# Kernel optimization log

Hardware: AMD Instinct MI355X
Metric: run time of the kernel (lower is better)

Reference implementation:

```python
import jax, jax.numpy as jnp
import numpy as np

WS = 7          # window_size
NH = 4          # num_heads
C = 128         # channels
N = WS * WS     # tokens per window = 49
BW = 4096       # number of windows total (batch * windows_per_image)
NW = 64         # windows per image (mask leading dim)


def _rel_pos_index(ws):
    coords = np.stack(np.meshgrid(np.arange(ws), np.arange(ws), indexing='ij'))
    cf = coords.reshape(2, -1)
    rel = (cf[:, :, None] - cf[:, None, :]).transpose(1, 2, 0)
    rel[:, :, 0] += ws - 1
    rel[:, :, 1] += ws - 1
    rel[:, :, 0] *= 2 * ws - 1
    return jnp.asarray(rel.sum(-1).ravel(), dtype=jnp.int32)  # [N*N]


def setup_inputs() -> dict:
    key = jax.random.key(0)
    ks = jax.random.split(key, 6)
    x = jax.random.normal(ks[0], (BW, N, C), dtype=jnp.float32)
    qkv_w = jax.random.normal(ks[1], (C, 3 * C), dtype=jnp.float32) * 0.02
    qkv_b = jnp.zeros((3 * C,), dtype=jnp.float32)
    proj_w = jax.random.normal(ks[2], (C, C), dtype=jnp.float32) * 0.02
    proj_b = jnp.zeros((C,), dtype=jnp.float32)
    bias_table = jax.random.normal(ks[3], ((2 * WS - 1) ** 2, NH), dtype=jnp.float32) * 0.02
    # Swin shifted-window mask: 0 where attention allowed, -100 where blocked
    keep = jax.random.bernoulli(ks[4], 0.5, (NW, N, N))
    mask = jnp.where(keep, 0.0, -100.0).astype(jnp.float32)
    return {"x": x, "qkv_w": qkv_w, "qkv_b": qkv_b, "proj_w": proj_w,
            "proj_b": proj_b, "bias_table": bias_table, "mask": mask}


def reference(x, qkv_w, qkv_b, proj_w, proj_b, bias_table, mask):
    B_, n, c = x.shape
    h = NH
    d = c // h
    scale = d ** -0.5

    qkv = x @ qkv_w + qkv_b                       # [B_, N, 3C]
    qkv = qkv.reshape(B_, n, 3, h, d).transpose(2, 0, 3, 1, 4)  # [3, B_, h, N, d]
    q, k, v = qkv[0], qkv[1], qkv[2]

    attn = jnp.einsum('bhnd,bhmd->bhnm', q * scale, k)          # [B_, h, N, N]

    idx = _rel_pos_index(WS)
    rpb = bias_table[idx].reshape(n, n, h).transpose(2, 0, 1)   # [h, N, N]
    attn = attn + rpb[None]

    nW = mask.shape[0]
    attn = attn.reshape(-1, nW, h, n, n) + mask[None, :, None]  # [B, nW, h, N, N]
    attn = attn.reshape(-1, h, n, n)
    attn = jax.nn.softmax(attn, axis=-1)

    out = jnp.einsum('bhnm,bhmd->bhnd', attn, v)  # [B_, h, N, d]
    out = out.transpose(0, 2, 1, 3).reshape(B_, n, c)
    return out @ proj_w + proj_b
```

## Files before the change

kernel.cpp:

```cpp
#include <hip/hip_runtime.h>

#define NTOK 49
#define CH   128
#define NHEAD 4
#define SCALE 0.17677669529663687f

typedef __bf16 bf16x8 __attribute__((ext_vector_type(8)));
typedef short  s16x8  __attribute__((ext_vector_type(8)));
typedef float  f32x4  __attribute__((ext_vector_type(4)));
typedef s16x8 s16x8_a __attribute__((may_alias));
typedef unsigned short u16_a __attribute__((may_alias));

__device__ __forceinline__ unsigned short f2bf(float f) {
  unsigned int u = __builtin_bit_cast(unsigned int, f);
  u += 0x7FFFu + ((u >> 16) & 1u);
  return (unsigned short)(u >> 16);
}

__device__ __forceinline__ f32x4 mfma_bf16(s16x8 a, s16x8 b, f32x4 c) {
  return __builtin_amdgcn_mfma_f32_16x16x32_bf16(
      __builtin_bit_cast(bf16x8, a), __builtin_bit_cast(bf16x8, b), c, 0, 0, 0);
}

__global__ void prep_kernel(const float* __restrict__ qkv_w,
                            const float* __restrict__ proj_w,
                            const float* __restrict__ bias_table,
                            unsigned short* __restrict__ wT,
                            unsigned short* __restrict__ pT,
                            float* __restrict__ rpb) {
  int t = blockIdx.x * 256 + threadIdx.x;
  if (t < 384 * 128) {
    int n = t >> 7, k = t & 127;
    float v = qkv_w[k * 384 + n];
    if (n < 128) v *= SCALE;
    wT[n * 128 + k] = f2bf(v);
  } else if (t < 384 * 128 + 128 * 128) {
    int u = t - 384 * 128;
    int n = u >> 7, k = u & 127;
    pT[n * 128 + k] = f2bf(proj_w[k * 128 + n]);
  } else if (t < 384 * 128 + 128 * 128 + NHEAD * NTOK * NTOK) {
    int u = t - (384 * 128 + 128 * 128);
    int h = u / (NTOK * NTOK);
    int ij = u % (NTOK * NTOK);
    int i = ij / NTOK, j = ij % NTOK;
    int idx = (i / 7 - j / 7 + 6) * 13 + (i % 7 - j % 7 + 6);
    rpb[h * (NTOK * NTOK) + ij] = bias_table[idx * NHEAD + h];
  }
}

__global__ __launch_bounds__(256, 3)
void attn_fused_kernel(const float* __restrict__ x,
                       const float* __restrict__ qkv_b,
                       const float* __restrict__ proj_b,
                       const float* __restrict__ mask,
                       const unsigned short* __restrict__ wT,
                       const unsigned short* __restrict__ pT,
                       const float* __restrict__ rpb,
                       float* __restrict__ out) {
  __shared__ __align__(16) char smem_raw[54272];
  unsigned short* const smem = (unsigned short*)smem_raw;

  const int w    = blockIdx.x;
  const int tid  = threadIdx.x;
  const int wave = tid >> 6;
  const int lane = tid & 63;
  const int quad = lane >> 4;
  const int l16  = lane & 15;
  const int h    = wave;
  const int wq8  = quad * 8;

  unsigned short* const Xs   = smem;
  unsigned short* const priv = smem + 6656 + wave * 5120;
  unsigned short* const qs   = priv;
  unsigned short* const ks   = priv + 2560;
  unsigned short* const ps   = priv;
  unsigned short* const vt   = priv + 2560;
  unsigned short* const ao   = smem;

  const f32x4 fzero = {0.f, 0.f, 0.f, 0.f};

  {
    const float* xw = x + (size_t)w * (NTOK * CH);
    for (int t = tid; t < NTOK * 32; t += 256) {
      const int row = t >> 5;
      const int c4  = (t & 31) << 2;
      const float4 v = *(const float4*)(xw + row * CH + c4);
      ushort4 pk;
      pk.x = f2bf(v.x); pk.y = f2bf(v.y); pk.z = f2bf(v.z); pk.w = f2bf(v.w);
      *(ushort4*)(Xs + row * 136 + c4) = pk;
    }
  }
  __syncthreads();

  int xrow[4];
#pragma unroll
  for (int mt = 0; mt < 4; ++mt) {
    const int rr = mt * 16 + l16;
    xrow[mt] = (rr < NTOK ? rr : NTOK - 1) * 136;
  }

  f32x4 accq[4][2], acck[4][2];
#pragma unroll
  for (int mt = 0; mt < 4; ++mt)
#pragma unroll
    for (int nt = 0; nt < 2; ++nt) { accq[mt][nt] = fzero; acck[mt][nt] = fzero; }
#pragma unroll
  for (int kt = 0; kt < 4; ++kt) {
    s16x8 a[4], bq[2], bk[2];
#pragma unroll
    for (int mt = 0; mt < 4; ++mt)
      a[mt] = *(const s16x8*)(Xs + xrow[mt] + kt * 32 + wq8);
#pragma unroll
    for (int nt = 0; nt < 2; ++nt) {
      const int rowq = h * 32 + nt * 16 + l16;
      bq[nt] = *(const s16x8*)(wT + (size_t)rowq * 128 + kt * 32 + wq8);
      bk[nt] = *(const s16x8*)(wT + (size_t)(128 + rowq) * 128 + kt * 32 + wq8);
    }
#pragma unroll
    for (int mt = 0; mt < 4; ++mt)
#pragma unroll
      for (int nt = 0; nt < 2; ++nt) {
        accq[mt][nt] = mfma_bf16(a[mt], bq[nt], accq[mt][nt]);
        acck[mt][nt] = mfma_bf16(a[mt], bk[nt], acck[mt][nt]);
      }
  }
#pragma unroll
  for (int nt = 0; nt < 2; ++nt) {
    const int col = nt * 16 + l16;
    const float bq_ = qkv_b[h * 32 + col] * SCALE;
    const float bk_ = qkv_b[128 + h * 32 + col];
#pragma unroll
    for (int mt = 0; mt < 4; ++mt)
#pragma unroll
      for (int r = 0; r < 4; ++r) {
        const int row = mt * 16 + quad * 4 + r;
        *(u16_a*)(qs + row * 40 + col) = f2bf(accq[mt][nt][r] + bq_);
        *(u16_a*)(ks + row * 40 + col) = f2bf(acck[mt][nt][r] + bk_);
      }
  }

  f32x4 accv[4][2];
#pragma unroll
  for (int mt = 0; mt < 4; ++mt)
#pragma unroll
    for (int nt = 0; nt < 2; ++nt) accv[mt][nt] = fzero;
#pragma unroll
  for (int kt = 0; kt < 4; ++kt) {
    s16x8 a[4], bv[2];
#pragma unroll
    for (int mt = 0; mt < 4; ++mt)
      a[mt] = *(const s16x8*)(Xs + xrow[mt] + kt * 32 + wq8);
#pragma unroll
    for (int nt = 0; nt < 2; ++nt)
      bv[nt] = *(const s16x8*)(wT + (size_t)(256 + h * 32 + nt * 16 + l16) * 128 + kt * 32 + wq8);
#pragma unroll
    for (int mt = 0; mt < 4; ++mt)
#pragma unroll
      for (int nt = 0; nt < 2; ++nt)
        accv[mt][nt] = mfma_bf16(a[mt], bv[nt], accv[mt][nt]);
  }

  s16x8 qf[4], kf[4];
#pragma unroll
  for (int t4 = 0; t4 < 4; ++t4) {
    qf[t4] = *(const s16x8_a*)(qs + (t4 * 16 + l16) * 40 + wq8);
    kf[t4] = *(const s16x8_a*)(ks + (t4 * 16 + l16) * 40 + wq8);
  }
  asm volatile("s_waitcnt lgkmcnt(0)" ::: "memory");

#pragma unroll
  for (int nt = 0; nt < 2; ++nt) {
    const float bv_ = qkv_b[256 + h * 32 + nt * 16 + l16];
#pragma unroll
    for (int mt = 0; mt < 4; ++mt)
#pragma unroll
      for (int r = 0; r < 4; ++r) {
        const int row = mt * 16 + quad * 4 + r;
        const int col = nt * 16 + l16;
        *(u16_a*)(vt + col * 72 + row) = f2bf(accv[mt][nt][r] + bv_);
      }
  }

  f32x4 s[4][4];
#pragma unroll
  for (int mt = 0; mt < 4; ++mt)
#pragma unroll
    for (int nt = 0; nt < 4; ++nt)
      s[mt][nt] = mfma_bf16(qf[mt], kf[nt], fzero);

  const float* maskw = mask + (size_t)(w & 63) * (NTOK * NTOK);
  const float* rpbh  = rpb + h * (NTOK * NTOK);
  float rinv[4][4];
  unsigned int pHold[4][4];
#pragma unroll
  for (int mt = 0; mt < 4; ++mt) {
#pragma unroll
    for (int r = 0; r < 4; ++r) {
      const int i = mt * 16 + quad * 4 + r;
      float vals[4];
      float vmax = -1e30f;
#pragma unroll
      for (int nt = 0; nt < 4; ++nt) {
        const int j = nt * 16 + l16;
        float v = -1e30f;
        if (i < NTOK && j < NTOK) {
          const int ij = i * NTOK + j;
          v = s[mt][nt][r] + rpbh[ij] + maskw[ij];
        }
        vals[nt] = v;
        vmax = fmaxf(vmax, v);
      }
#pragma unroll
      for (int off = 1; off < 16; off <<= 1)
        vmax = fmaxf(vmax, __shfl_xor(vmax, off, 64));
      float rsum = 0.f;
#pragma unroll
      for (int nt = 0; nt < 4; ++nt) {
        const float e = __expf(vals[nt] - vmax);
        vals[nt] = e;
        rsum += e;
      }
#pragma unroll
      for (int off = 1; off < 16; off <<= 1)
        rsum += __shfl_xor(rsum, off, 64);
      rinv[mt][r] = 1.f / rsum;
      *(u16_a*)(ps + i * 40 + l16)      = f2bf(vals[0]);
      *(u16_a*)(ps + i * 40 + 16 + l16) = f2bf(vals[1]);
      pHold[mt][r] = (unsigned int)f2bf(vals[2]) | ((unsigned int)f2bf(vals[3]) << 16);
    }
  }

  f32x4 o[4][2];
#pragma unroll
  for (int mt = 0; mt < 4; ++mt)
#pragma unroll
    for (int nt = 0; nt < 2; ++nt) o[mt][nt] = fzero;
  {
    s16x8 pf[4], vf[2];
#pragma unroll
    for (int mt = 0; mt < 4; ++mt)
      pf[mt] = *(const s16x8_a*)(ps + (mt * 16 + l16) * 40 + wq8);
#pragma unroll
    for (int nt = 0; nt < 2; ++nt)
      vf[nt] = *(const s16x8_a*)(vt + (nt * 16 + l16) * 72 + wq8);
#pragma unroll
    for (int mt = 0; mt < 4; ++mt)
#pragma unroll
      for (int nt = 0; nt < 2; ++nt)
        o[mt][nt] = mfma_bf16(pf[mt], vf[nt], o[mt][nt]);
  }
  asm volatile("" ::: "memory");
#pragma unroll
  for (int mt = 0; mt < 4; ++mt)
#pragma unroll
    for (int r = 0; r < 4; ++r) {
      const int i = mt * 16 + quad * 4 + r;
      *(u16_a*)(ps + i * 40 + l16)      = (unsigned short)(pHold[mt][r] & 0xFFFFu);
      *(u16_a*)(ps + i * 40 + 16 + l16) = (unsigned short)(pHold[mt][r] >> 16);
    }
  asm volatile("" ::: "memory");
  {
    s16x8 pf[4], vf[2];
#pragma unroll
    for (int mt = 0; mt < 4; ++mt)
      pf[mt] = *(const s16x8_a*)(ps + (mt * 16 + l16) * 40 + wq8);
#pragma unroll
    for (int nt = 0; nt < 2; ++nt)
      vf[nt] = *(const s16x8_a*)(vt + (nt * 16 + l16) * 72 + 32 + wq8);
#pragma unroll
    for (int mt = 0; mt < 4; ++mt)
#pragma unroll
      for (int nt = 0; nt < 2; ++nt)
        o[mt][nt] = mfma_bf16(pf[mt], vf[nt], o[mt][nt]);
  }

  __syncthreads();
#pragma unroll
  for (int mt = 0; mt < 4; ++mt)
#pragma unroll
    for (int nt = 0; nt < 2; ++nt)
#pragma unroll
      for (int r = 0; r < 4; ++r) {
        const int row = mt * 16 + quad * 4 + r;
        *(u16_a*)(ao + row * 136 + h * 32 + nt * 16 + l16) = f2bf(o[mt][nt][r] * rinv[mt][r]);
      }
  __syncthreads();

  f32x4 po[4][2];
#pragma unroll
  for (int mt = 0; mt < 4; ++mt)
#pragma unroll
    for (int nt = 0; nt < 2; ++nt) po[mt][nt] = fzero;
#pragma unroll
  for (int kt = 0; kt < 4; ++kt) {
    s16x8 a[4], b[2];
#pragma unroll
    for (int mt = 0; mt < 4; ++mt)
      a[mt] = *(const s16x8_a*)(ao + (mt * 16 + l16) * 136 + kt * 32 + wq8);
#pragma unroll
    for (int nt = 0; nt < 2; ++nt)
      b[nt] = *(const s16x8*)(pT + (size_t)(h * 32 + nt * 16 + l16) * 128 + kt * 32 + wq8);
#pragma unroll
    for (int mt = 0; mt < 4; ++mt)
#pragma unroll
      for (int nt = 0; nt < 2; ++nt)
        po[mt][nt] = mfma_bf16(a[mt], b[nt], po[mt][nt]);
  }
  float* outw = out + (size_t)w * (NTOK * CH);
#pragma unroll
  for (int nt = 0; nt < 2; ++nt) {
    const int col = h * 32 + nt * 16 + l16;
    const float pb = proj_b[col];
#pragma unroll
    for (int mt = 0; mt < 4; ++mt)
#pragma unroll
      for (int r = 0; r < 4; ++r) {
        const int row = mt * 16 + quad * 4 + r;
        if (row < NTOK) outw[row * CH + col] = po[mt][nt][r] + pb;
      }
  }
}

extern "C" void kernel_launch(void* const* d_in, const int* in_sizes, int n_in,
                              void* d_out, int out_size, void* d_ws, size_t ws_size,
                              hipStream_t stream) {
  (void)in_sizes; (void)n_in; (void)out_size; (void)ws_size;
  const float* x          = (const float*)d_in[0];
  const float* qkv_w      = (const float*)d_in[1];
  const float* qkv_b      = (const float*)d_in[2];
  const float* proj_w     = (const float*)d_in[3];
  const float* proj_b     = (const float*)d_in[4];
  const float* bias_table = (const float*)d_in[5];
  const float* mask       = (const float*)d_in[6];
  float* out = (float*)d_out;

  unsigned short* wT = (unsigned short*)d_ws;
  unsigned short* pT = wT + 384 * 128;
  float* rpb = (float*)(pT + 128 * 128);

  const int prep_items = 384 * 128 + 128 * 128 + NHEAD * NTOK * NTOK;
  prep_kernel<<<(prep_items + 255) / 256, 256, 0, stream>>>(qkv_w, proj_w, bias_table,
                                                            wT, pT, rpb);
  attn_fused_kernel<<<4096, 256, 0, stream>>>(x, qkv_b, proj_b, mask, wT, pT, rpb, out);
}
```

Baseline: 323.2 us.

## Compute Q and K projections sequentially sharing one LDS staging buffer

Splits the fused Q/K projection loop into two passes. Q is staged through LDS and read into registers first, then K reuses the same LDS region, so each wave's private scratch shrinks and the block's shared memory drops. It also lowers peak accumulator register pressure, since only one set of accumulators is live at a time. Explicit waitcnt and sched_barrier calls are added to order LDS reuse safely, which serialises some work and limits scheduler overlap.

```diff
diff --git a/kernel.cpp b/kernel.cpp
--- a/kernel.cpp
+++ b/kernel.cpp
@@ -57,7 +57,7 @@
                        const unsigned short* __restrict__ pT,
                        const float* __restrict__ rpb,
                        float* __restrict__ out) {
-  __shared__ __align__(16) char smem_raw[54272];
+  __shared__ __align__(16) char smem_raw[52224];
   unsigned short* const smem = (unsigned short*)smem_raw;
 
   const int w    = blockIdx.x;
@@ -70,9 +70,9 @@
   const int wq8  = quad * 8;
 
   unsigned short* const Xs   = smem;
-  unsigned short* const priv = smem + 6656 + wave * 5120;
+  unsigned short* const priv = smem + 6656 + wave * 4864;
   unsigned short* const qs   = priv;
-  unsigned short* const ks   = priv + 2560;
+  unsigned short* const ks   = priv;
   unsigned short* const ps   = priv;
   unsigned short* const vt   = priv + 2560;
   unsigned short* const ao   = smem;
@@ -99,45 +99,81 @@
     xrow[mt] = (rr < NTOK ? rr : NTOK - 1) * 136;
   }
 
-  f32x4 accq[4][2], acck[4][2];
-#pragma unroll
-  for (int mt = 0; mt < 4; ++mt)
-#pragma unroll
-    for (int nt = 0; nt < 2; ++nt) { accq[mt][nt] = fzero; acck[mt][nt] = fzero; }
+  f32x4 accq[4][2];
+#pragma unroll
+  for (int mt = 0; mt < 4; ++mt)
+#pragma unroll
+    for (int nt = 0; nt < 2; ++nt) accq[mt][nt] = fzero;
 #pragma unroll
   for (int kt = 0; kt < 4; ++kt) {
-    s16x8 a[4], bq[2], bk[2];
+    s16x8 a[4], bq[2];
 #pragma unroll
     for (int mt = 0; mt < 4; ++mt)
       a[mt] = *(const s16x8*)(Xs + xrow[mt] + kt * 32 + wq8);
 #pragma unroll
-    for (int nt = 0; nt < 2; ++nt) {
-      const int rowq = h * 32 + nt * 16 + l16;
-      bq[nt] = *(const s16x8*)(wT + (size_t)rowq * 128 + kt * 32 + wq8);
-      bk[nt] = *(const s16x8*)(wT + (size_t)(128 + rowq) * 128 + kt * 32 + wq8);
-    }
-#pragma unroll
-    for (int mt = 0; mt < 4; ++mt)
-#pragma unroll
-      for (int nt = 0; nt < 2; ++nt) {
+    for (int nt = 0; nt < 2; ++nt)
+      bq[nt] = *(const s16x8*)(wT + (size_t)(h * 32 + nt * 16 + l16) * 128 + kt * 32 + wq8);
+#pragma unroll
+    for (int mt = 0; mt < 4; ++mt)
+#pragma unroll
+      for (int nt = 0; nt < 2; ++nt)
         accq[mt][nt] = mfma_bf16(a[mt], bq[nt], accq[mt][nt]);
-        acck[mt][nt] = mfma_bf16(a[mt], bk[nt], acck[mt][nt]);
-      }
   }
 #pragma unroll
   for (int nt = 0; nt < 2; ++nt) {
     const int col = nt * 16 + l16;
     const float bq_ = qkv_b[h * 32 + col] * SCALE;
+#pragma unroll
+    for (int mt = 0; mt < 4; ++mt)
+#pragma unroll
+      for (int r = 0; r < 4; ++r)
+        *(u16_a*)(qs + (mt * 16 + quad * 4 + r) * 40 + col) = f2bf(accq[mt][nt][r] + bq_);
+  }
+  asm volatile("" ::: "memory");
+  s16x8 qf[4];
+#pragma unroll
+  for (int t4 = 0; t4 < 4; ++t4)
+    qf[t4] = *(const s16x8_a*)(qs + (t4 * 16 + l16) * 40 + wq8);
+  asm volatile("s_waitcnt lgkmcnt(0)" ::: "memory");
+  __builtin_amdgcn_sched_barrier(0);
+
+  f32x4 acck[4][2];
+#pragma unroll
+  for (int mt = 0; mt < 4; ++mt)
+#pragma unroll
+    for (int nt = 0; nt < 2; ++nt) acck[mt][nt] = fzero;
+#pragma unroll
+  for (int kt = 0; kt < 4; ++kt) {
+    s16x8 a[4], bk[2];
+#pragma unroll
+    for (int mt = 0; mt < 4; ++mt)
+      a[mt] = *(const s16x8*)(Xs + xrow[mt] + kt * 32 + wq8);
+#pragma unroll
+    for (int nt = 0; nt < 2; ++nt)
+      bk[nt] = *(const s16x8*)(wT + (size_t)(128 + h * 32 + nt * 16 + l16) * 128 + kt * 32 + wq8);
+#pragma unroll
+    for (int mt = 0; mt < 4; ++mt)
+#pragma unroll
+      for (int nt = 0; nt < 2; ++nt)
+        acck[mt][nt] = mfma_bf16(a[mt], bk[nt], acck[mt][nt]);
+  }
+#pragma unroll
+  for (int nt = 0; nt < 2; ++nt) {
+    const int col = nt * 16 + l16;
     const float bk_ = qkv_b[128 + h * 32 + col];
 #pragma unroll
     for (int mt = 0; mt < 4; ++mt)
 #pragma unroll
-      for (int r = 0; r < 4; ++r) {
-        const int row = mt * 16 + quad * 4 + r;
-        *(u16_a*)(qs + row * 40 + col) = f2bf(accq[mt][nt][r] + bq_);
-        *(u16_a*)(ks + row * 40 + col) = f2bf(acck[mt][nt][r] + bk_);
-      }
-  }
+      for (int r = 0; r < 4; ++r)
+        *(u16_a*)(ks + (mt * 16 + quad * 4 + r) * 40 + col) = f2bf(acck[mt][nt][r] + bk_);
+  }
+  asm volatile("" ::: "memory");
+  s16x8 kf[4];
+#pragma unroll
+  for (int t4 = 0; t4 < 4; ++t4)
+    kf[t4] = *(const s16x8_a*)(ks + (t4 * 16 + l16) * 40 + wq8);
+  asm volatile("s_waitcnt lgkmcnt(0)" ::: "memory");
+  __builtin_amdgcn_sched_barrier(0);
 
   f32x4 accv[4][2];
 #pragma unroll
@@ -159,15 +195,6 @@
       for (int nt = 0; nt < 2; ++nt)
         accv[mt][nt] = mfma_bf16(a[mt], bv[nt], accv[mt][nt]);
   }
-
-  s16x8 qf[4], kf[4];
-#pragma unroll
-  for (int t4 = 0; t4 < 4; ++t4) {
-    qf[t4] = *(const s16x8_a*)(qs + (t4 * 16 + l16) * 40 + wq8);
-    kf[t4] = *(const s16x8_a*)(ks + (t4 * 16 + l16) * 40 + wq8);
-  }
-  asm volatile("s_waitcnt lgkmcnt(0)" ::: "memory");
-
 #pragma unroll
   for (int nt = 0; nt < 2; ++nt) {
     const float bv_ = qkv_b[256 + h * 32 + nt * 16 + l16];
@@ -249,7 +276,8 @@
       for (int nt = 0; nt < 2; ++nt)
         o[mt][nt] = mfma_bf16(pf[mt], vf[nt], o[mt][nt]);
   }
-  asm volatile("" ::: "memory");
+  asm volatile("s_waitcnt lgkmcnt(0)" ::: "memory");
+  __builtin_amdgcn_sched_barrier(0);
 #pragma unroll
   for (int mt = 0; mt < 4; ++mt)
 #pragma unroll
```

Result: faster. 294.8 us (-8.8%).
